# Kernel optimization log

Measured on AMD Instinct MI355X. Metric: run time of the kernel, lower is better.

Reference implementation:

```python
import jax, jax.numpy as jnp
import numpy as np

B, S, D, H = 2, 2048, 1024, 16
HD = D // H  # 64
MASK_VAL = -10000.0


def setup_inputs() -> dict:
    key = jax.random.key(0)
    ks = jax.random.split(key, 8)
    sc = 0.02
    q_features = jax.random.normal(ks[0], (B, S, D), jnp.float32)
    kv_features = jax.random.normal(ks[1], (B, S, D), jnp.float32)
    # causal mask, broadcastable (1,1,S,S)
    mask = jnp.tril(jnp.ones((S, S), jnp.bool_))[None, None]
    Wq = jax.random.normal(ks[2], (D, D), jnp.float32) * sc
    bq = jnp.zeros((D,), jnp.float32)
    Wkv = jax.random.normal(ks[3], (D, 2 * D), jnp.float32) * sc
    bkv = jnp.zeros((2 * D,), jnp.float32)
    Wp = jax.random.normal(ks[4], (D, D), jnp.float32) * sc
    bp = jnp.zeros((D,), jnp.float32)
    return {"q_features": q_features, "kv_features": kv_features, "mask": mask,
            "Wq": Wq, "bq": bq, "Wkv": Wkv, "bkv": bkv, "Wp": Wp, "bp": bp}


def _split_heads(t):
    # (B,S,D) -> (B,H,S,HD)
    return t.reshape(B, S, H, HD).transpose(0, 2, 1, 3)


def reference(q_features, kv_features, mask, Wq, bq, Wkv, bkv, Wp, bp):
    query = q_features @ Wq + bq            # (B,S,D)
    kv = kv_features @ Wkv + bkv            # (B,S,2D)
    key, value = jnp.split(kv, 2, axis=-1)
    q = _split_heads(query)                 # (B,H,S,HD)
    k = _split_heads(key)
    v = _split_heads(value)
    scores = jnp.einsum('bhqd,bhkd->bhqk', q, k) / jnp.sqrt(jnp.float32(HD))
    scores = jnp.where(mask, scores, jnp.asarray(MASK_VAL, scores.dtype))
    attn = jax.nn.softmax(scores, axis=-1)  # (B,H,S,S)
    out = jnp.einsum('bhqk,bhkd->bhqd', attn, v)
    out = out.transpose(0, 2, 1, 3).reshape(B, S, D)  # merge heads
    return out @ Wp + bp
```

## Files before the change

kernel.cpp:

```cpp
#include <hip/hip_runtime.h>

typedef unsigned short u16;
typedef unsigned int u32;
typedef __attribute__((ext_vector_type(4))) unsigned short us4;
typedef __attribute__((ext_vector_type(8))) unsigned short us8;
typedef __attribute__((ext_vector_type(4))) short s16x4;
typedef __attribute__((ext_vector_type(8))) __bf16 bf16x8;
typedef __attribute__((ext_vector_type(4))) float floatx4;

#define S_ 2048
#define D_ 1024
#define QSC 0.18033688f

__device__ __forceinline__ float b2f(u16 u) {
  unsigned v = ((unsigned)u) << 16;
  return __builtin_bit_cast(float, v);
}
__device__ __forceinline__ u16 f2bf(float f) {
  unsigned u = __builtin_bit_cast(unsigned, f);
  unsigned r = (u + 0x7fffu + ((u >> 16) & 1u)) >> 16;
  return (u16)r;
}
__device__ __forceinline__ u16 f2bf_rhu(float f) {
  return (u16)((__builtin_bit_cast(unsigned, f) + 0x8000u) >> 16);
}

typedef const __attribute__((address_space(1))) u32* gas_t;
typedef __attribute__((address_space(3))) u32* las_t;
__device__ __forceinline__ void gload16(const u16* g, u16* l) {
  __builtin_amdgcn_global_load_lds((gas_t)g, (las_t)l, 16, 0, 0);
}

#define PBAR()                                   \
  {                                              \
    __builtin_amdgcn_sched_barrier(0);           \
    asm volatile("" ::: "memory");               \
    __builtin_amdgcn_s_barrier();                \
    asm volatile("" ::: "memory");               \
    __builtin_amdgcn_sched_barrier(0);           \
  }
#define WAITVM(N) asm volatile("s_waitcnt vmcnt(" #N ")" ::: "memory")

__global__ __launch_bounds__(256) void prep(
    const float* __restrict__ qf, const float* __restrict__ kvf,
    const float* __restrict__ Wq, const float* __restrict__ Wkv,
    const float* __restrict__ Wp, u16* __restrict__ qa, u16* __restrict__ kva,
    u16* __restrict__ Wqt, u16* __restrict__ Wkvt, u16* __restrict__ Wpt) {
  int bid = blockIdx.x, tid = threadIdx.x;
  if (bid < 4096) {
    const float* src = (bid < 2048) ? qf : kvf;
    u16* dst = (bid < 2048) ? qa : kva;
    size_t i = ((size_t)(bid & 2047) * 256 + tid) * 8;
    floatx4 a = *(const floatx4*)(src + i);
    floatx4 b = *(const floatx4*)(src + i + 4);
    us8 r;
#pragma unroll
    for (int j = 0; j < 4; j++) { r[j] = f2bf(a[j]); r[4 + j] = f2bf(b[j]); }
    *(us8*)(dst + i) = r;
  } else {
    int t = bid - 4096;
    const float* src; u16* dst; int R, C;
    if (t < 1024)      { src = Wq;  dst = Wqt;  R = 1024; C = 1024; }
    else if (t < 3072) { t -= 1024; src = Wkv; dst = Wkvt; R = 1024; C = 2048; }
    else               { t -= 3072; src = Wp;  dst = Wpt;  R = 1024; C = 1024; }
    int bx = t % (C >> 5), by = t / (C >> 5);
    __shared__ u16 tile[32][33];
    int tx = tid & 31, ty = tid >> 5;
    int x = bx * 32 + tx;
    for (int i = ty; i < 32; i += 8)
      tile[i][tx] = f2bf(src[(size_t)(by * 32 + i) * C + x]);
    __syncthreads();
    int r = tid >> 3, c4 = tid & 7;
    us4 v;
#pragma unroll
    for (int j = 0; j < 4; j++) v[j] = tile[c4 * 4 + j][r];
    *(us4*)&dst[(size_t)(bx * 32 + r) * R + by * 32 + c4 * 4] = v;
  }
}

template <int MODE>
__device__ __forceinline__ void gemm256(
    const u16* __restrict__ A, const u16* __restrict__ Bt,
    const float* __restrict__ bias, void* __restrict__ C0,
    u16* __restrict__ C1, int N, int m0, int n0, u16* smem, float cscale) {
  int tid = threadIdx.x;
  int w = tid >> 6, lane = tid & 63;
  int quad = lane >> 4, l16 = lane & 15;
  int wr = w >> 2, wc = w & 3;

  int srow = w * 32 + (lane >> 2);
  int gchunk = ((lane & 3) ^ ((lane >> 3) & 3)) << 3;
  const u16* Asrc = A + (size_t)(m0 + srow) * 1024 + gchunk;
  const u16* Bsrc = Bt + (size_t)(n0 + srow) * 1024 + gchunk;
  u16* Adst = smem + w * 1024;
  u16* Bdst = smem + 32768 + w * 1024;

  int swz = (quad ^ ((l16 >> 1) & 3)) << 3;
  int aoff = (wr * 128 + l16) * 32 + swz;
  int boff = 32768 + (wc * 64 + l16) * 32 + swz;

  floatx4 acc[8][4] = {};

#define STG(t)                                                 \
  {                                                            \
    int s_ = (t) & 3;                                          \
    gload16(Asrc + (t) * 32, Adst + s_ * 8192);                \
    gload16(Asrc + (t) * 32 + 16384, Adst + s_ * 8192 + 512);  \
    gload16(Bsrc + (t) * 32, Bdst + s_ * 8192);                \
    gload16(Bsrc + (t) * 32 + 16384, Bdst + s_ * 8192 + 512);  \
  }

  STG(0); STG(1); STG(2);
  WAITVM(8);
  PBAR();

#pragma unroll 1
  for (int t = 0; t < 32; t++) {
    int so = (t & 3) * 8192;
    bf16x8 af[8], bf[4];
#pragma unroll
    for (int mf = 0; mf < 8; mf++)
      af[mf] = __builtin_bit_cast(bf16x8,
          *(const us8*)&smem[so + aoff + mf * 512]);
#pragma unroll
    for (int nf = 0; nf < 4; nf++)
      bf[nf] = __builtin_bit_cast(bf16x8,
          *(const us8*)&smem[so + boff + nf * 512]);
    if (t < 29) STG(t + 3);
    __builtin_amdgcn_s_setprio(1);
#pragma unroll
    for (int mf = 0; mf < 8; mf++)
#pragma unroll
      for (int nf = 0; nf < 4; nf++)
        acc[mf][nf] = __builtin_amdgcn_mfma_f32_16x16x32_bf16(
            af[mf], bf[nf], acc[mf][nf], 0, 0, 0);
    __builtin_amdgcn_s_setprio(0);
    if (t < 29)      { WAITVM(8); }
    else if (t == 29){ WAITVM(4); }
    else if (t == 30){ WAITVM(0); }
    if (t < 31) PBAR();
  }
#undef STG

#pragma unroll
  for (int mf = 0; mf < 8; mf++) {
#pragma unroll
    for (int nf = 0; nf < 4; nf++) {
      int col = n0 + wc * 64 + nf * 16 + l16;
      int rowq = m0 + wr * 128 + mf * 16 + quad * 4;
      float bv = bias[col];
      if (MODE == 0) {
        u16* o = (u16*)C0;
#pragma unroll
        for (int r = 0; r < 4; r++)
          o[(size_t)(rowq + r) * N + col] = f2bf((acc[mf][nf][r] + bv) * cscale);
      } else {
        if (col < 1024) {
          u16* o = (u16*)C0;
#pragma unroll
          for (int r = 0; r < 4; r++)
            o[(size_t)(rowq + r) * 1024 + col] = f2bf(acc[mf][nf][r] + bv);
        } else {
          int vcol = col - 1024;
          int b = rowq >> 11, s0 = rowq & 2047;
          us4 pv;
#pragma unroll
          for (int r = 0; r < 4; r++) pv[r] = f2bf(acc[mf][nf][r] + bv);
          *(us4*)&C1[((size_t)(b * 1024 + vcol)) * (size_t)S_ + s0] = pv;
        }
      }
    }
  }
}

__global__ __launch_bounds__(512, 2) void gemm_qkv(
    const u16* __restrict__ qa, const u16* __restrict__ kva,
    const u16* __restrict__ Wqt, const u16* __restrict__ Wkvt,
    const float* __restrict__ bq, const float* __restrict__ bkv,
    u16* __restrict__ Qb, u16* __restrict__ Kb, u16* __restrict__ Vt) {
  __shared__ __align__(16) u16 smem[65536];
  int bid = blockIdx.x;
  int work = (bid & 7) * 24 + (bid >> 3);
  if (work < 64) {
    gemm256<0>(qa, Wqt, bq, Qb, nullptr, 1024,
               (work >> 2) * 256, (work & 3) * 256, smem, QSC);
  } else {
    int lb = work - 64;
    gemm256<2>(kva, Wkvt, bkv, Kb, Vt, 2048,
               (lb >> 3) * 256, (lb & 7) * 256, smem, 1.0f);
  }
}

template <int TM, int TN, int MODE>
__device__ __forceinline__ void gemm4w(
    const u16* __restrict__ A, const u16* __restrict__ Bt,
    const float* __restrict__ bias, void* __restrict__ C0,
    u16* __restrict__ C1, int N, int m0, int n0, u16* smem, float cscale) {
  constexpr int MF = TM / 32, NF = TN / 32;
  constexpr int ASZ = TM * 64;
  constexpr int SLOT = (TM + TN) * 64;
  int tid = threadIdx.x;
  int w = tid >> 6, lane = tid & 63;
  int quad = lane >> 4, l16 = lane & 15;
  int wr = w >> 1, wc = w & 1;

  int gch = ((lane & 7) ^ ((lane >> 3) & 7)) << 3;
  const u16* Ag = A + (size_t)(m0 + w * (TM / 4) + (lane >> 3)) * 1024 + gch;
  const u16* Bg = Bt + (size_t)(n0 + w * (TN / 4) + (lane >> 3)) * 1024 + gch;
  u16* Adst = smem + w * (TM / 4) * 64;
  u16* Bdst = smem + ASZ + w * (TN / 4) * 64;

  int ab = (wr * (TM / 2) + l16) * 64;
  int bb = ASZ + (wc * (TN / 2) + l16) * 64;
  int xk0 = (quad ^ (l16 & 7)) << 3;
  int xk1 = ((4 + quad) ^ (l16 & 7)) << 3;

  floatx4 acc[MF][NF] = {};

#define STAGE4(tn, s_)                                                  \
  {                                                                     \
    _Pragma("unroll") for (int i = 0; i < MF; i++)                      \
      gload16(Ag + (size_t)(tn) * 64 + (size_t)i * 8192,                \
              Adst + (s_) * SLOT + i * 512);                            \
    _Pragma("unroll") for (int i = 0; i < NF; i++)                      \
      gload16(Bg + (size_t)(tn) * 64 + (size_t)i * 8192,                \
              Bdst + (s_) * SLOT + i * 512);                            \
  }

#define COMPUTE4(SOFF)                                                  \
  {                                                                     \
    _Pragma("unroll") for (int kk = 0; kk < 2; kk++) {                  \
      int xk = kk ? xk1 : xk0;                                          \
      bf16x8 bfr[NF];                                                   \
      _Pragma("unroll") for (int nf = 0; nf < NF; nf++)                 \
        bfr[nf] = __builtin_bit_cast(bf16x8,                            \
            *(const us8*)&smem[(SOFF) + bb + nf * 1024 + xk]);          \
      _Pragma("unroll") for (int mf = 0; mf < MF; mf++) {               \
        bf16x8 afr = __builtin_bit_cast(bf16x8,                         \
            *(const us8*)&smem[(SOFF) + ab + mf * 1024 + xk]);          \
        _Pragma("unroll") for (int nf = 0; nf < NF; nf++)               \
          acc[mf][nf] = __builtin_amdgcn_mfma_f32_16x16x32_bf16(        \
              afr, bfr[nf], acc[mf][nf], 0, 0, 0);                      \
      }                                                                 \
    }                                                                   \
  }

  STAGE4(0, 0);
  WAITVM(0);
  PBAR();
#pragma unroll 1
  for (int t = 0; t < 16; t += 2) {
    STAGE4(t + 1, 1);
    COMPUTE4(0);
    WAITVM(0);
    PBAR();
    if (t + 2 < 16) STAGE4(t + 2, 0);
    COMPUTE4(SLOT);
    WAITVM(0);
    PBAR();
  }

#undef STAGE4
#undef COMPUTE4

#pragma unroll
  for (int mf = 0; mf < MF; mf++) {
#pragma unroll
    for (int nf = 0; nf < NF; nf++) {
      int col = n0 + wc * (TN / 2) + nf * 16 + l16;
      int rowq = m0 + wr * (TM / 2) + mf * 16 + quad * 4;
      float bv = bias[col];
      if (MODE == 0) {
        u16* o = (u16*)C0;
#pragma unroll
        for (int r = 0; r < 4; r++)
          o[(size_t)(rowq + r) * N + col] = f2bf((acc[mf][nf][r] + bv) * cscale);
      } else if (MODE == 1) {
        float* o = (float*)C0;
#pragma unroll
        for (int r = 0; r < 4; r++)
          o[(size_t)(rowq + r) * N + col] = acc[mf][nf][r] + bv;
      } else {
        if (col < 1024) {
          u16* o = (u16*)C0;
#pragma unroll
          for (int r = 0; r < 4; r++)
            o[(size_t)(rowq + r) * 1024 + col] = f2bf(acc[mf][nf][r] + bv);
        } else {
          int vcol = col - 1024;
          int b = rowq >> 11, s0 = rowq & 2047;
          us4 pv;
#pragma unroll
          for (int r = 0; r < 4; r++) pv[r] = f2bf(acc[mf][nf][r] + bv);
          *(us4*)&C1[((size_t)(b * 1024 + vcol)) * (size_t)S_ + s0] = pv;
        }
      }
    }
  }
}

__global__ __launch_bounds__(256, 3) void gemm_out(
    const u16* __restrict__ AO, const u16* __restrict__ Wpt,
    const float* __restrict__ bp, float* __restrict__ out) {
  __shared__ __align__(16) u16 smem[24576];
  int work = (blockIdx.x & 7) * 64 + (blockIdx.x >> 3);
  gemm4w<128, 64, 1>(AO, Wpt, bp, out, nullptr, 1024,
                     (work >> 4) * 128, (work & 15) * 64, smem, 1.0f);
}

__global__ __launch_bounds__(512) void attn_fwd(
    const u16* __restrict__ Q, const u16* __restrict__ Kb,
    const u16* __restrict__ Vt, u16* __restrict__ O,
    u16* __restrict__ Opart, float* __restrict__ ml) {
  __shared__ __align__(16) u16 sm[16384];
  int tid  = threadIdx.x;
  int w    = tid >> 6, lane = tid & 63;
  int quad = lane >> 4, l16 = lane & 15;
  int bh = blockIdx.x, b = bh >> 4, h = bh & 15;
  int y = blockIdx.y;

  static const signed char yt_[24] = {15,15,7,14,14,13,13,6,12,12,11,11,5,
                                      10,10,9,9,4,8,8,3,2,1,0};
  static const signed char yh_[24] = {0,1,-1,0,1,0,1,-1,0,1,0,1,-1,
                                      0,1,0,1,-1,0,1,-1,-1,-1,-1};
  int t = yt_[y], hh = yh_[y];
  bool split = hh >= 0;
  int kb0, kb1;
  if (split) { kb0 = hh ? (t + 1) : 0; kb1 = hh ? (2 * t + 2) : (t + 1); }
  else       { kb0 = 0; kb1 = 2 * t + 2; }
  int n = kb1 - kb0;

  const size_t row0 = (size_t)b * S_;
  const u16* Kg = Kb + row0 * D_ + h * 64;
  const u16* Vg = Vt + ((size_t)b * 1024 + h * 64) * S_;

  int qlo = t * 128 + w * 16;
  int dkb = qlo >> 6;
  int qg  = (qlo & 63) + l16;

  const u16* qp = Q + (row0 + qlo + l16) * D_ + h * 64 + quad * 8;
  bf16x8 aqv[2];
  aqv[0] = __builtin_bit_cast(bf16x8, *(const us8*)(qp));
  aqv[1] = __builtin_bit_cast(bf16x8, *(const us8*)(qp + 32));

  floatx4 o_[4] = {};
  floatx4 l_acc = {};
  const s16x4 ones4 = {0x3F80, 0x3F80, 0x3F80, 0x3F80};

  int srow = tid >> 3, c8 = tid & 7;
  int woff = srow * 64 + ((c8 ^ (srow & 7)) << 3);
  u16* smK = sm;
  u16* smV = sm + 8192;

  const u16* Kp = Kg + (size_t)(kb0 * 64 + srow) * D_ + c8 * 8;
  const u16* Vp = Vg + (size_t)srow * S_ + kb0 * 64 + c8 * 8;
  us8 pk = *(const us8*)Kp, pv = *(const us8*)Vp;
  *(us8*)&smK[woff] = pk;
  *(us8*)&smV[woff] = pv;
  if (n > 1) {
    Kp += (size_t)64 * D_; Vp += 64;
    pk = *(const us8*)Kp; pv = *(const us8*)Vp;
  }
  __syncthreads();

  for (int i = 0; i < n; i++) {
    int cur = i & 1;
    int kb = kb0 + i;
    if (i + 1 < n) {
      int nxt = (cur ^ 1) * 4096;
      *(us8*)&smK[nxt + woff] = pk;
      *(us8*)&smV[nxt + woff] = pv;
      if (i + 2 < n) {
        Kp += (size_t)64 * D_; Vp += 64;
        pk = *(const us8*)Kp; pv = *(const us8*)Vp;
      }
    }
    if (kb <= dkb) {
      const u16* Ksb = smK + cur * 4096;
      const u16* Vsb = smV + cur * 4096;

      floatx4 s[4] = {};
      __builtin_amdgcn_s_setprio(1);
#pragma unroll
      for (int kk = 0; kk < 2; kk++)
#pragma unroll
        for (int nt = 0; nt < 4; nt++) {
          us8 kf = *(const us8*)&Ksb[(nt * 16 + l16) * 64 +
                                     (((kk * 4 + quad) ^ (l16 & 7)) << 3)];
          s[nt] = __builtin_amdgcn_mfma_f32_16x16x32_bf16(
              __builtin_bit_cast(bf16x8, kf), aqv[kk], s[nt], 0, 0, 0);
        }
      __builtin_amdgcn_s_setprio(0);

      if (kb == dkb) {
#pragma unroll
        for (int nt = 0; nt < 4; nt++)
#pragma unroll
          for (int r = 0; r < 4; r++)
            if (nt * 16 + quad * 4 + r > qg) s[nt][r] = -1e5f;
      }

      s16x4 pb[4];
#pragma unroll
      for (int nt = 0; nt < 4; nt++)
#pragma unroll
        for (int r = 0; r < 4; r++)
          pb[nt][r] = (short)f2bf_rhu(__builtin_amdgcn_exp2f(s[nt][r]));

      __builtin_amdgcn_s_setprio(1);
#pragma unroll
      for (int nt = 0; nt < 4; nt++) {
        l_acc = __builtin_amdgcn_mfma_f32_16x16x16bf16_1k(ones4, pb[nt], l_acc, 0, 0, 0);
#pragma unroll
        for (int mt = 0; mt < 4; mt++) {
          int hd = mt * 16 + l16;
          int chunk = nt * 2 + (quad >> 1);
          us4 vf = *(const us4*)&Vsb[hd * 64 + ((chunk ^ (l16 & 7)) << 3) + (quad & 1) * 4];
          o_[mt] = __builtin_amdgcn_mfma_f32_16x16x16bf16_1k(
              __builtin_bit_cast(s16x4, vf), pb[nt], o_[mt], 0, 0, 0);
        }
      }
      __builtin_amdgcn_s_setprio(0);
    }
    __syncthreads();
  }

  if (!split) {
    float rl = __builtin_amdgcn_rcpf(l_acc[0]);
    size_t orow = (row0 + qlo + l16) * D_ + h * 64;
#pragma unroll
    for (int mt = 0; mt < 4; mt++) {
      us4 ov;
#pragma unroll
      for (int r = 0; r < 4; r++) ov[r] = f2bf(o_[mt][r] * rl);
      *(us4*)&O[orow + mt * 16 + quad * 4] = ov;
    }
  } else {
    int part = (t - 8) * 2 + hh;
    u16* op = Opart + ((size_t)(bh * 16 + part)) * 8192;
    int rloc = w * 16 + l16;
#pragma unroll
    for (int mt = 0; mt < 4; mt++) {
      us4 ov;
#pragma unroll
      for (int r = 0; r < 4; r++) ov[r] = f2bf(o_[mt][r]);
      *(us4*)&op[rloc * 64 + mt * 16 + quad * 4] = ov;
    }
    if (quad == 0)
      ml[(size_t)(bh * 16 + part) * 128 + rloc] = l_acc[0];
  }
}

__global__ __launch_bounds__(256) void combine(
    const u16* __restrict__ Opart, const float* __restrict__ ml,
    u16* __restrict__ O) {
  int bh = blockIdx.x, b = bh >> 4, h = bh & 15;
  int t = 8 + blockIdx.y;
  int p0 = bh * 16 + (t - 8) * 2;
  const u16* o1 = Opart + (size_t)p0 * 8192;
  const u16* o2 = o1 + 8192;
  int row = threadIdx.x >> 1, ch = (threadIdx.x & 1) * 32;
  float l1 = ml[(size_t)p0 * 128 + row];
  float l2 = ml[(size_t)(p0 + 1) * 128 + row];
  float inv = __builtin_amdgcn_rcpf(l1 + l2);
  size_t orow = ((size_t)b * S_ + t * 128 + row) * D_ + h * 64 + ch;
#pragma unroll
  for (int v = 0; v < 4; v++) {
    us8 x1 = *(const us8*)&o1[row * 64 + ch + v * 8];
    us8 x2 = *(const us8*)&o2[row * 64 + ch + v * 8];
    us8 out;
#pragma unroll
    for (int j = 0; j < 8; j++)
      out[j] = f2bf((b2f(x1[j]) + b2f(x2[j])) * inv);
    *(us8*)&O[orow + v * 8] = out;
  }
}

extern "C" void kernel_launch(void* const* d_in, const int* in_sizes, int n_in,
                              void* d_out, int out_size, void* d_ws, size_t ws_size,
                              hipStream_t stream) {
  const float* qf  = (const float*)d_in[0];
  const float* kvf = (const float*)d_in[1];
  const float* Wq  = (const float*)d_in[3];
  const float* bq  = (const float*)d_in[4];
  const float* Wkv = (const float*)d_in[5];
  const float* bkv = (const float*)d_in[6];
  const float* Wp  = (const float*)d_in[7];
  const float* bp  = (const float*)d_in[8];

  char* ws = (char*)d_ws;
  const size_t MB = 1048576;
  u16*   kva  = (u16*)(ws);
  u16*   AO   = (u16*)(ws);
  u16*   Kbp  = (u16*)(ws + 8 * MB);
  u16*   Vtp  = (u16*)(ws + 16 * MB);
  u16*   Wqt  = (u16*)(ws + 24 * MB);
  float* mlp  = (float*)(ws + 24 * MB);
  u16*   Wkvt = (u16*)(ws + 26 * MB);
  u16*   Wpt  = (u16*)(ws + 30 * MB);
  u16*   qa    = (u16*)d_out;
  u16*   Opart = (u16*)d_out;
  u16*   Qb    = (u16*)d_out + (size_t)4 * 1048576;

  prep<<<8192, 256, 0, stream>>>(qf, kvf, Wq, Wkv, Wp, qa, kva, Wqt, Wkvt, Wpt);
  gemm_qkv<<<192, 512, 0, stream>>>(qa, kva, Wqt, Wkvt, bq, bkv, Qb, Kbp, Vtp);
  attn_fwd<<<dim3(32, 24), 512, 0, stream>>>(Qb, Kbp, Vtp, AO, Opart, mlp);
  combine<<<dim3(32, 8), 256, 0, stream>>>(Opart, mlp, AO);
  gemm_out<<<512, 256, 0, stream>>>(AO, Wpt, bp, (float*)d_out);
}
```

Measured before the change: 207.3 us.

## Process 32 query rows per wave in attention, halving block threads

The attention kernel now runs 4 waves of 256 threads instead of 8 waves. Each wave handles 32 query rows as two 16-row halves, so every K and V fragment read from shared memory feeds two MFMAs. Each thread loads two K/V rows into shared memory to keep the 128-row query tile per block. The aim is to halve LDS reads per unit of MFMA work. The cost is more registers per thread and fewer waves per block to hide latency.

```diff
diff --git a/kernel.cpp b/kernel.cpp
--- a/kernel.cpp
+++ b/kernel.cpp
@@ -308,7 +308,7 @@
                      (work >> 4) * 128, (work & 15) * 64, smem, 1.0f);
 }
 
-__global__ __launch_bounds__(512) void attn_fwd(
+__global__ __launch_bounds__(256) void attn_fwd(
     const u16* __restrict__ Q, const u16* __restrict__ Kb,
     const u16* __restrict__ Vt, u16* __restrict__ O,
     u16* __restrict__ Opart, float* __restrict__ ml) {
@@ -334,17 +334,19 @@
   const u16* Kg = Kb + row0 * D_ + h * 64;
   const u16* Vg = Vt + ((size_t)b * 1024 + h * 64) * S_;
 
-  int qlo = t * 128 + w * 16;
+  int qlo = t * 128 + w * 32;
   int dkb = qlo >> 6;
-  int qg  = (qlo & 63) + l16;
+  int qgb = (w & 1) * 32;
 
   const u16* qp = Q + (row0 + qlo + l16) * D_ + h * 64 + quad * 8;
-  bf16x8 aqv[2];
-  aqv[0] = __builtin_bit_cast(bf16x8, *(const us8*)(qp));
-  aqv[1] = __builtin_bit_cast(bf16x8, *(const us8*)(qp + 32));
-
-  floatx4 o_[4] = {};
-  floatx4 l_acc = {};
+  bf16x8 aq[2][2];
+  aq[0][0] = __builtin_bit_cast(bf16x8, *(const us8*)(qp));
+  aq[0][1] = __builtin_bit_cast(bf16x8, *(const us8*)(qp + 32));
+  aq[1][0] = __builtin_bit_cast(bf16x8, *(const us8*)(qp + (size_t)16 * D_));
+  aq[1][1] = __builtin_bit_cast(bf16x8, *(const us8*)(qp + (size_t)16 * D_ + 32));
+
+  floatx4 o_[2][4] = {};
+  floatx4 l_acc[2] = {};
   const s16x4 ones4 = {0x3F80, 0x3F80, 0x3F80, 0x3F80};
 
   int srow = tid >> 3, c8 = tid & 7;
@@ -354,12 +356,14 @@
 
   const u16* Kp = Kg + (size_t)(kb0 * 64 + srow) * D_ + c8 * 8;
   const u16* Vp = Vg + (size_t)srow * S_ + kb0 * 64 + c8 * 8;
-  us8 pk = *(const us8*)Kp, pv = *(const us8*)Vp;
-  *(us8*)&smK[woff] = pk;
-  *(us8*)&smV[woff] = pv;
+  us8 pk0 = *(const us8*)Kp, pk1 = *(const us8*)(Kp + (size_t)32 * D_);
+  us8 pv0 = *(const us8*)Vp, pv1 = *(const us8*)(Vp + (size_t)32 * S_);
+  *(us8*)&smK[woff] = pk0; *(us8*)&smK[woff + 2048] = pk1;
+  *(us8*)&smV[woff] = pv0; *(us8*)&smV[woff + 2048] = pv1;
   if (n > 1) {
     Kp += (size_t)64 * D_; Vp += 64;
-    pk = *(const us8*)Kp; pv = *(const us8*)Vp;
+    pk0 = *(const us8*)Kp; pk1 = *(const us8*)(Kp + (size_t)32 * D_);
+    pv0 = *(const us8*)Vp; pv1 = *(const us8*)(Vp + (size_t)32 * S_);
   }
   __syncthreads();
 
@@ -368,18 +372,19 @@
     int kb = kb0 + i;
     if (i + 1 < n) {
       int nxt = (cur ^ 1) * 4096;
-      *(us8*)&smK[nxt + woff] = pk;
-      *(us8*)&smV[nxt + woff] = pv;
+      *(us8*)&smK[nxt + woff] = pk0; *(us8*)&smK[nxt + woff + 2048] = pk1;
+      *(us8*)&smV[nxt + woff] = pv0; *(us8*)&smV[nxt + woff + 2048] = pv1;
       if (i + 2 < n) {
         Kp += (size_t)64 * D_; Vp += 64;
-        pk = *(const us8*)Kp; pv = *(const us8*)Vp;
+        pk0 = *(const us8*)Kp; pk1 = *(const us8*)(Kp + (size_t)32 * D_);
+        pv0 = *(const us8*)Vp; pv1 = *(const us8*)(Vp + (size_t)32 * S_);
       }
     }
     if (kb <= dkb) {
       const u16* Ksb = smK + cur * 4096;
       const u16* Vsb = smV + cur * 4096;
 
-      floatx4 s[4] = {};
+      floatx4 s[2][4] = {};
       __builtin_amdgcn_s_setprio(1);
 #pragma unroll
       for (int kk = 0; kk < 2; kk++)
@@ -387,37 +392,50 @@
         for (int nt = 0; nt < 4; nt++) {
           us8 kf = *(const us8*)&Ksb[(nt * 16 + l16) * 64 +
                                      (((kk * 4 + quad) ^ (l16 & 7)) << 3)];
-          s[nt] = __builtin_amdgcn_mfma_f32_16x16x32_bf16(
-              __builtin_bit_cast(bf16x8, kf), aqv[kk], s[nt], 0, 0, 0);
+          bf16x8 kfb = __builtin_bit_cast(bf16x8, kf);
+          s[0][nt] = __builtin_amdgcn_mfma_f32_16x16x32_bf16(
+              kfb, aq[0][kk], s[0][nt], 0, 0, 0);
+          s[1][nt] = __builtin_amdgcn_mfma_f32_16x16x32_bf16(
+              kfb, aq[1][kk], s[1][nt], 0, 0, 0);
         }
       __builtin_amdgcn_s_setprio(0);
 
       if (kb == dkb) {
 #pragma unroll
+        for (int hf = 0; hf < 2; hf++) {
+          int qg = qgb + hf * 16 + l16;
+#pragma unroll
+          for (int nt = 0; nt < 4; nt++)
+#pragma unroll
+            for (int r = 0; r < 4; r++)
+              if (nt * 16 + quad * 4 + r > qg) s[hf][nt][r] = -1e5f;
+        }
+      }
+
+      s16x4 pb[2][4];
+#pragma unroll
+      for (int hf = 0; hf < 2; hf++)
+#pragma unroll
         for (int nt = 0; nt < 4; nt++)
 #pragma unroll
           for (int r = 0; r < 4; r++)
-            if (nt * 16 + quad * 4 + r > qg) s[nt][r] = -1e5f;
-      }
-
-      s16x4 pb[4];
-#pragma unroll
-      for (int nt = 0; nt < 4; nt++)
-#pragma unroll
-        for (int r = 0; r < 4; r++)
-          pb[nt][r] = (short)f2bf_rhu(__builtin_amdgcn_exp2f(s[nt][r]));
+            pb[hf][nt][r] = (short)f2bf_rhu(__builtin_amdgcn_exp2f(s[hf][nt][r]));
 
       __builtin_amdgcn_s_setprio(1);
 #pragma unroll
       for (int nt = 0; nt < 4; nt++) {
-        l_acc = __builtin_amdgcn_mfma_f32_16x16x16bf16_1k(ones4, pb[nt], l_acc, 0, 0, 0);
+        l_acc[0] = __builtin_amdgcn_mfma_f32_16x16x16bf16_1k(ones4, pb[0][nt], l_acc[0], 0, 0, 0);
+        l_acc[1] = __builtin_amdgcn_mfma_f32_16x16x16bf16_1k(ones4, pb[1][nt], l_acc[1], 0, 0, 0);
 #pragma unroll
         for (int mt = 0; mt < 4; mt++) {
           int hd = mt * 16 + l16;
           int chunk = nt * 2 + (quad >> 1);
           us4 vf = *(const us4*)&Vsb[hd * 64 + ((chunk ^ (l16 & 7)) << 3) + (quad & 1) * 4];
-          o_[mt] = __builtin_amdgcn_mfma_f32_16x16x16bf16_1k(
-              __builtin_bit_cast(s16x4, vf), pb[nt], o_[mt], 0, 0, 0);
+          s16x4 vb = __builtin_bit_cast(s16x4, vf);
+          o_[0][mt] = __builtin_amdgcn_mfma_f32_16x16x16bf16_1k(
+              vb, pb[0][nt], o_[0][mt], 0, 0, 0);
+          o_[1][mt] = __builtin_amdgcn_mfma_f32_16x16x16bf16_1k(
+              vb, pb[1][nt], o_[1][mt], 0, 0, 0);
         }
       }
       __builtin_amdgcn_s_setprio(0);
@@ -426,28 +444,34 @@
   }
 
   if (!split) {
-    float rl = __builtin_amdgcn_rcpf(l_acc[0]);
-    size_t orow = (row0 + qlo + l16) * D_ + h * 64;
-#pragma unroll
-    for (int mt = 0; mt < 4; mt++) {
-      us4 ov;
-#pragma unroll
-      for (int r = 0; r < 4; r++) ov[r] = f2bf(o_[mt][r] * rl);
-      *(us4*)&O[orow + mt * 16 + quad * 4] = ov;
+#pragma unroll
+    for (int hf = 0; hf < 2; hf++) {
+      float rl = __builtin_amdgcn_rcpf(l_acc[hf][0]);
+      size_t orow = (row0 + qlo + hf * 16 + l16) * D_ + h * 64;
+#pragma unroll
+      for (int mt = 0; mt < 4; mt++) {
+        us4 ov;
+#pragma unroll
+        for (int r = 0; r < 4; r++) ov[r] = f2bf(o_[hf][mt][r] * rl);
+        *(us4*)&O[orow + mt * 16 + quad * 4] = ov;
+      }
     }
   } else {
     int part = (t - 8) * 2 + hh;
     u16* op = Opart + ((size_t)(bh * 16 + part)) * 8192;
-    int rloc = w * 16 + l16;
-#pragma unroll
-    for (int mt = 0; mt < 4; mt++) {
-      us4 ov;
-#pragma unroll
-      for (int r = 0; r < 4; r++) ov[r] = f2bf(o_[mt][r]);
-      *(us4*)&op[rloc * 64 + mt * 16 + quad * 4] = ov;
+#pragma unroll
+    for (int hf = 0; hf < 2; hf++) {
+      int rloc = w * 32 + hf * 16 + l16;
+#pragma unroll
+      for (int mt = 0; mt < 4; mt++) {
+        us4 ov;
+#pragma unroll
+        for (int r = 0; r < 4; r++) ov[r] = f2bf(o_[hf][mt][r]);
+        *(us4*)&op[rloc * 64 + mt * 16 + quad * 4] = ov;
+      }
+      if (quad == 0)
+        ml[(size_t)(bh * 16 + part) * 128 + rloc] = l_acc[hf][0];
     }
-    if (quad == 0)
-      ml[(size_t)(bh * 16 + part) * 128 + rloc] = l_acc[0];
   }
 }
 
@@ -504,7 +528,7 @@
 
   prep<<<8192, 256, 0, stream>>>(qf, kvf, Wq, Wkv, Wp, qa, kva, Wqt, Wkvt, Wpt);
   gemm_qkv<<<192, 512, 0, stream>>>(qa, kva, Wqt, Wkvt, bq, bkv, Qb, Kbp, Vtp);
-  attn_fwd<<<dim3(32, 24), 512, 0, stream>>>(Qb, Kbp, Vtp, AO, Opart, mlp);
+  attn_fwd<<<dim3(32, 24), 256, 0, stream>>>(Qb, Kbp, Vtp, AO, Opart, mlp);
   combine<<<dim3(32, 8), 256, 0, stream>>>(Opart, mlp, AO);
   gemm_out<<<512, 256, 0, stream>>>(AO, Wpt, bp, (float*)d_out);
 }
```

New measurement: 212.3 us. 2.4% more time.
